# Optimization experiments

Measured on AMD Instinct MI355X. Metric: run time of the kernel, lower is better.

Reference implementation:

```python
import jax, jax.numpy as jnp
import numpy as np

N, E, IN, TD, H, C0, C1 = 50000, 800000, 128, 64, 4, 64, 16
SLOPE = 0.2


def setup_inputs() -> dict:
    key = jax.random.key(0)
    ks = jax.random.split(key, 20)
    def rn(k, shape, scale=1.0):
        return jax.random.normal(k, shape, dtype=jnp.float32) * scale
    return {
        "x": rn(ks[0], (N, IN)),
        "edge_index": jax.random.randint(ks[1], (2, E), 0, N),
        "timestamps": jax.random.uniform(ks[2], (E,), dtype=jnp.float32),
        # TimeEncoder: linear(1 -> TD) then cos, then abs
        "time_w": rn(ks[3], (TD,)),
        "time_b": rn(ks[4], (TD,)),
        # GATConv layer 0: in=IN, out-per-head=C0, heads=H
        "W0": rn(ks[5], (IN, H * C0), 0.1),
        "att_src0": rn(ks[6], (H, C0), 0.1),
        "att_dst0": rn(ks[7], (H, C0), 0.1),
        "lin_edge0": rn(ks[8], (TD, H * C0), 0.1),
        "att_edge0": rn(ks[9], (H, C0), 0.1),
        "bias0": rn(ks[10], (H * C0,), 0.1),
        # GATConv layer 1: in=H*C0, out-per-head=C1, heads=H
        "W1": rn(ks[11], (H * C0, H * C1), 0.1),
        "att_src1": rn(ks[12], (H, C1), 0.1),
        "att_dst1": rn(ks[13], (H, C1), 0.1),
        "lin_edge1": rn(ks[14], (TD, H * C1), 0.1),
        "att_edge1": rn(ks[15], (H, C1), 0.1),
        "bias1": rn(ks[16], (H * C1,), 0.1),
    }


def gat_layer(h_in, src, dst, edge_attr, W, a_src, a_dst, W_e, a_e, bias):
    """One PyG-style GATConv with edge-attr attention (concat heads, no dropout)."""
    heads = a_src.shape[0]
    HC = W.shape[1]
    C = HC // heads
    n_nodes = h_in.shape[0]
    h = (h_in @ W).reshape(n_nodes, heads, C)                 # [N, H, C]
    e = (edge_attr @ W_e).reshape(-1, heads, C)               # [Et, H, C]
    # attention logits per edge, per head
    alpha = ((h * a_src).sum(-1)[src]
             + (h * a_dst).sum(-1)[dst]
             + (e * a_e).sum(-1))                              # [Et, H]
    alpha = jnp.where(alpha >= 0, alpha, SLOPE * alpha)       # leaky relu
    # segment softmax over destination node
    m = jax.ops.segment_max(alpha, dst, num_segments=n_nodes)  # [N, H]
    ea = jnp.exp(alpha - m[dst])
    s = jax.ops.segment_sum(ea, dst, num_segments=n_nodes)
    a = ea / (s[dst] + 1e-16)                                 # [Et, H]
    # weighted scatter-add aggregation
    out = jax.ops.segment_sum(h[src] * a[..., None], dst, num_segments=n_nodes)
    return out.reshape(n_nodes, HC) + bias


def reference(x, edge_index, timestamps, time_w, time_b,
              W0, att_src0, att_dst0, lin_edge0, att_edge0, bias0,
              W1, att_src1, att_dst1, lin_edge1, att_edge1, bias1):
    # TimeEncoder -> abs, per-edge feature [E, TD]
    ef = jnp.abs(jnp.cos(timestamps[:, None] * time_w + time_b))
    # add self loops with edge_attr fill value 1.0
    loops = jnp.arange(N)
    src = jnp.concatenate([edge_index[0], loops])
    dst = jnp.concatenate([edge_index[1], loops])
    ef = jnp.concatenate([ef, jnp.ones((N, TD), ef.dtype)], axis=0)
    h = gat_layer(x, src, dst, ef, W0, att_src0, att_dst0, lin_edge0, att_edge0, bias0)
    h = gat_layer(h, src, dst, ef, W1, att_src1, att_dst1, lin_edge1, att_edge1, bias1)
    return h  # [N, H*C1] = [50000, 64]
```

## Files before the change

### kernel.cpp

```cpp
#include <hip/hip_runtime.h>
#include <math.h>

#define N_NODES 50000
#define N_EDGES 800000
#define ET (N_EDGES + N_NODES)
#define IN_F 128
#define TDIM 64
#define HEADS 4
#define C0 64
#define C1 16
#define HC0 256
#define HC1 64
#define KF 512
#define SLOPE 0.2f
#define TAB 4096
#define BSHIFT 7
#define NBUCKET 391
#define CHUNK 2048

using short8 = __attribute__((ext_vector_type(8))) short;
using f32x4 = __attribute__((ext_vector_type(4))) float;

__device__ __forceinline__ float bf2f(unsigned u16) { return __uint_as_float(u16 << 16); }
__device__ __forceinline__ unsigned short f2bf(float f) {
    unsigned u = __float_as_uint(f);
    return (unsigned short)((u + 0x7fffu + ((u >> 16) & 1u)) >> 16);
}
__device__ __forceinline__ unsigned pk2(float lo, float hi) {
    return (unsigned)f2bf(lo) | ((unsigned)f2bf(hi) << 16);
}
__device__ __forceinline__ float lrelu(float a) { return a >= 0.f ? a : SLOPE * a; }

__global__ __launch_bounds__(256) void k_param(
    const float* __restrict__ le0, const float* __restrict__ at0, const float* __restrict__ le1,
    const float* __restrict__ at1, const float* __restrict__ W0, const float* __restrict__ asr,
    const float* __restrict__ ads, const float* __restrict__ W1, const float* __restrict__ bias0,
    const float* __restrict__ asr1, const float* __restrict__ ads1,
    const float* __restrict__ tw, const float* __restrict__ tb, float* __restrict__ l0,
    float* __restrict__ l1, float* __restrict__ as0, float* __restrict__ ad0,
    unsigned short* __restrict__ W01t, float* __restrict__ b01, float* __restrict__ as1,
    float* __restrict__ ad1, float* __restrict__ bs1, float* __restrict__ bd1,
    float* __restrict__ tab0, float* __restrict__ tab1) {
    int b = blockIdx.x, tid = threadIdx.x;
    int h = tid >> 6, c = tid & 63;
    if (b == 0) {
        float s0 = 0.f;
        for (int td = 0; td < TDIM; ++td) s0 += le0[td * HC0 + h * C0 + c];
        s0 *= at0[h * C0 + c];
        for (int m = 1; m < 64; m <<= 1) s0 += __shfl_xor(s0, m);
        if (c == 0) l0[h] = s0;
        float s1 = 0.f;
        if (c < C1) {
            for (int td = 0; td < TDIM; ++td) s1 += le1[td * HC1 + h * C1 + c];
            s1 *= at1[h * C1 + c];
        }
        for (int m = 1; m < 16; m <<= 1) s1 += __shfl_xor(s1, m);
        if (c == 0) l1[h] = s1;
    } else if (b < 129) {
        int k = b - 1;
        float wv = W0[k * HC0 + h * C0 + c];
        float ps = wv * asr[h * C0 + c];
        float pd = wv * ads[h * C0 + c];
        for (int m = 1; m < 64; m <<= 1) {
            ps += __shfl_xor(ps, m);
            pd += __shfl_xor(pd, m);
        }
        if (c == 0) {
            as0[h * IN_F + k] = ps;
            ad0[h * IN_F + k] = pd;
        }
    } else if (b < 257) {
        int hk = (b - 129) * 4 + (tid >> 6);
        int c1 = tid & 63;
        int hh = hk >> 7, k = hk & 127;
        float acc = 0.f;
        for (int c0 = 0; c0 < C0; ++c0)
            acc += W0[k * HC0 + hh * C0 + c0] * W1[(size_t)(hh * C0 + c0) * HC1 + c1];
        W01t[(size_t)c1 * KF + hk] = f2bf(acc);
        float ps = acc * asr1[c1];
        float pd = acc * ads1[c1];
        for (int m = 1; m < 16; m <<= 1) {
            ps += __shfl_xor(ps, m);
            pd += __shfl_xor(pd, m);
        }
        if ((c1 & 15) == 0) {
            as1[(c1 >> 4) * KF + hk] = ps;
            ad1[(c1 >> 4) * KF + hk] = pd;
        }
    } else if (b == 257) {
        if (tid < 64) {
            float acc = 0.f;
            for (int k = 0; k < HC0; ++k) acc += bias0[k] * W1[(size_t)k * HC1 + tid];
            b01[tid] = acc;
            float ps = acc * asr1[tid];
            float pd = acc * ads1[tid];
            for (int m = 1; m < 16; m <<= 1) {
                ps += __shfl_xor(ps, m);
                pd += __shfl_xor(pd, m);
            }
            if ((tid & 15) == 0) {
                bs1[tid >> 4] = ps;
                bd1[tid >> 4] = pd;
            }
        }
    } else {
        __shared__ float sv0[TDIM * 4], sv1[TDIM * 4], sw[TDIM], sb[TDIM];
        int td = tid >> 2, hh = tid & 3;
        float v0l = 0.f;
        for (int c0 = 0; c0 < C0; ++c0) v0l += le0[td * HC0 + hh * C0 + c0] * at0[hh * C0 + c0];
        sv0[td * 4 + hh] = v0l;
        float v1l = 0.f;
        for (int c0 = 0; c0 < C1; ++c0) v1l += le1[td * HC1 + hh * C1 + c0] * at1[hh * C1 + c0];
        sv1[td * 4 + hh] = v1l;
        if (tid < TDIM) {
            sw[tid] = tw[tid];
            sb[tid] = tb[tid];
        }
        __syncthreads();
        int i = (b - 258) * 256 + tid;
        if (i > TAB) return;
        float time = (float)i / (float)TAB;
        float a00 = 0, a01 = 0, a02 = 0, a03 = 0, a10 = 0, a11 = 0, a12 = 0, a13 = 0;
#pragma unroll 8
        for (int d = 0; d < TDIM; ++d) {
            float f = fabsf(__cosf(time * sw[d] + sb[d]));
            a00 += f * sv0[d * 4 + 0];
            a01 += f * sv0[d * 4 + 1];
            a02 += f * sv0[d * 4 + 2];
            a03 += f * sv0[d * 4 + 3];
            a10 += f * sv1[d * 4 + 0];
            a11 += f * sv1[d * 4 + 1];
            a12 += f * sv1[d * 4 + 2];
            a13 += f * sv1[d * 4 + 3];
        }
        ((float4*)tab0)[i] = make_float4(a00, a01, a02, a03);
        ((float4*)tab1)[i] = make_float4(a10, a11, a12, a13);
    }
}

__global__ __launch_bounds__(256) void k_xbs(const float* __restrict__ x,
                                             const float* __restrict__ as0,
                                             const float* __restrict__ ad0,
                                             unsigned short* __restrict__ xb,
                                             float* __restrict__ ssrc, float* __restrict__ sdst,
                                             int* __restrict__ deg) {
    if (blockIdx.x < 196) {
        int i = blockIdx.x * 256 + threadIdx.x;
        if (i < N_NODES) deg[i] = 0;
    }
    int w = threadIdx.x >> 6, l = threadIdx.x & 63;
    int n = blockIdx.x * 4 + w;
    if (n >= N_NODES) return;
    float2 xv = *(const float2*)(x + (size_t)n * IN_F + l * 2);
    *(unsigned*)(xb + (size_t)n * IN_F + l * 2) = pk2(xv.x, xv.y);
    float ps[4], pd[4];
#pragma unroll
    for (int h = 0; h < 4; ++h) {
        float2 a = *(const float2*)(as0 + h * IN_F + l * 2);
        float2 d = *(const float2*)(ad0 + h * IN_F + l * 2);
        ps[h] = xv.x * a.x + xv.y * a.y;
        pd[h] = xv.x * d.x + xv.y * d.y;
    }
#pragma unroll
    for (int m = 1; m < 64; m <<= 1) {
#pragma unroll
        for (int h = 0; h < 4; ++h) {
            ps[h] += __shfl_xor(ps[h], m);
            pd[h] += __shfl_xor(pd[h], m);
        }
    }
    if (l == 0) {
#pragma unroll
        for (int h = 0; h < 4; ++h) {
            ssrc[n * 4 + h] = ps[h];
            sdst[n * 4 + h] = pd[h];
        }
    }
}

__global__ void k_count(const int* __restrict__ ei, int* __restrict__ deg) {
    int t = blockIdx.x * blockDim.x + threadIdx.x;
    if (t >= N_EDGES) return;
    atomicAdd(&deg[ei[N_EDGES + t]], 1);
}

__global__ void k_scan_block(const int* __restrict__ deg, int* __restrict__ rowptr,
                             int* __restrict__ blocksum, int n) {
    __shared__ int buf[256];
    int tid = threadIdx.x, i = blockIdx.x * 256 + tid;
    int v = (i < n) ? (deg[i] + 1) : 0;
    buf[tid] = v;
    __syncthreads();
    for (int off = 1; off < 256; off <<= 1) {
        int t = (tid >= off) ? buf[tid - off] : 0;
        __syncthreads();
        buf[tid] += t;
        __syncthreads();
    }
    if (i < n) rowptr[i + 1] = buf[tid];
    if (tid == 255) blocksum[blockIdx.x] = buf[255];
}

__global__ void k_scan_top(const int* __restrict__ blocksum, int* __restrict__ blockoff, int nb) {
    __shared__ int buf[256];
    int tid = threadIdx.x;
    int v = (tid < nb) ? blocksum[tid] : 0;
    buf[tid] = v;
    __syncthreads();
    for (int off = 1; off < 256; off <<= 1) {
        int t = (tid >= off) ? buf[tid - off] : 0;
        __syncthreads();
        buf[tid] += t;
        __syncthreads();
    }
    if (tid < nb) blockoff[tid] = buf[tid] - v;
}

__global__ void k_finalize(int* __restrict__ rowptr, const int* __restrict__ blockoff,
                           const int* __restrict__ deg, int* __restrict__ cursor,
                           int* __restrict__ edst, int* __restrict__ esrc,
                           float* __restrict__ tsp, int* __restrict__ bcur,
                           const float* __restrict__ ssrc0, const float* __restrict__ sdst0,
                           const float* __restrict__ l0, float* __restrict__ ew0p) {
    int i = blockIdx.x * 256 + threadIdx.x;
    if (i >= N_NODES) return;
    int v = rowptr[i + 1] + blockoff[blockIdx.x];
    rowptr[i + 1] = v;
    int start = v - deg[i] - 1;
    cursor[i] = start;
    if (i == 0) rowptr[0] = 0;
    if ((i & ((1 << BSHIFT) - 1)) == 0) bcur[i >> BSHIFT] = start;
    for (int p = start; p < v; ++p) edst[p] = i;
    esrc[v - 1] = i;
    tsp[v - 1] = -1.f;
    float4 lv = ((const float4*)l0)[0];
    float4 sv = ((const float4*)ssrc0)[i];
    float4 dv = ((const float4*)sdst0)[i];
    float4 w;
    w.x = __expf(lrelu(sv.x + dv.x + lv.x));
    w.y = __expf(lrelu(sv.y + dv.y + lv.y));
    w.z = __expf(lrelu(sv.z + dv.z + lv.z));
    w.w = __expf(lrelu(sv.w + dv.w + lv.w));
    ((float4*)ew0p)[v - 1] = w;
}

__global__ __launch_bounds__(256) void k_bucketA(const int* __restrict__ ei,
                                                 const float* __restrict__ ts,
                                                 int* __restrict__ bcur,
                                                 int4* __restrict__ staging) {
    __shared__ int cnt[NBUCKET], base[NBUCKET];
    int tid = threadIdx.x;
    int e0 = blockIdx.x * CHUNK;
    for (int i = tid; i < NBUCKET; i += 256) cnt[i] = 0;
    __syncthreads();
    int s[8], d[8], tv[8];
#pragma unroll
    for (int i = 0; i < 8; ++i) {
        int tt = e0 + i * 256 + tid;
        if (tt < N_EDGES) {
            s[i] = ei[tt];
            d[i] = ei[N_EDGES + tt];
            tv[i] = __float_as_int(ts[tt]);
            atomicAdd(&cnt[d[i] >> BSHIFT], 1);
        } else {
            d[i] = -1;
        }
    }
    __syncthreads();
    for (int i = tid; i < NBUCKET; i += 256) {
        int c = cnt[i];
        base[i] = c ? atomicAdd(&bcur[i], c) : 0;
        cnt[i] = 0;
    }
    __syncthreads();
#pragma unroll
    for (int i = 0; i < 8; ++i) {
        if (d[i] >= 0) {
            int b = d[i] >> BSHIFT;
            int off = atomicAdd(&cnt[b], 1);
            staging[base[b] + off] = make_int4(s[i], d[i], tv[i], 0);
        }
    }
}

__global__ __launch_bounds__(256) void k_bucketB(
    const int* __restrict__ rowptr, const int* __restrict__ bcur,
    const int4* __restrict__ staging, int* __restrict__ cursor, int* __restrict__ esrc,
    float* __restrict__ tsp, const float* __restrict__ ssrc0, const float* __restrict__ sdst0,
    const float* __restrict__ tab0, float* __restrict__ ew0p) {
    int b = blockIdx.x;
    int lo = rowptr[b << BSHIFT];
    int hi = bcur[b];
    for (int p = lo + threadIdx.x; p < hi; p += 256) {
        int4 sdt = staging[p];
        int q = atomicAdd(&cursor[sdt.y], 1);
        esrc[q] = sdt.x;
        float tv = __int_as_float(sdt.z);
        tsp[q] = tv;
        float f = tv * (float)TAB;
        int i = (int)f;
        i = i > TAB - 1 ? TAB - 1 : i;
        float fr = f - (float)i;
        float4 t0 = ((const float4*)tab0)[i];
        float4 t1 = ((const float4*)tab0)[i + 1];
        float4 sv = ((const float4*)ssrc0)[sdt.x];
        float4 dv = ((const float4*)sdst0)[sdt.y];
        float4 w;
        w.x = __expf(lrelu(sv.x + dv.x + t0.x + fr * (t1.x - t0.x)));
        w.y = __expf(lrelu(sv.y + dv.y + t0.y + fr * (t1.y - t0.y)));
        w.z = __expf(lrelu(sv.z + dv.z + t0.z + fr * (t1.z - t0.z)));
        w.w = __expf(lrelu(sv.w + dv.w + t0.w + fr * (t1.w - t0.w)));
        ((float4*)ew0p)[q] = w;
    }
}

__global__ void k_ew1(const int* __restrict__ esrc, const int* __restrict__ edst,
                      const float* __restrict__ tsp, const float* __restrict__ tab1,
                      const float* __restrict__ l1, const float* __restrict__ ssrc,
                      const float* __restrict__ sdst, float* __restrict__ ew1p) {
    int p = blockIdx.x * blockDim.x + threadIdx.x;
    if (p >= ET) return;
    float tv = tsp[p];
    float4 av;
    if (tv < 0.f) {
        av = ((const float4*)l1)[0];
    } else {
        float f = tv * (float)TAB;
        int i = (int)f;
        i = i > TAB - 1 ? TAB - 1 : i;
        float fr = f - (float)i;
        float4 t0 = ((const float4*)tab1)[i];
        float4 t1 = ((const float4*)tab1)[i + 1];
        av.x = t0.x + fr * (t1.x - t0.x);
        av.y = t0.y + fr * (t1.y - t0.y);
        av.z = t0.z + fr * (t1.z - t0.z);
        av.w = t0.w + fr * (t1.w - t0.w);
    }
    int s = esrc[p], d = edst[p];
    float4 sv = ((const float4*)ssrc)[s];
    float4 dv = ((const float4*)sdst)[d];
    float4 w;
    w.x = __expf(lrelu(sv.x + dv.x + av.x));
    w.y = __expf(lrelu(sv.y + dv.y + av.y));
    w.z = __expf(lrelu(sv.z + dv.z + av.z));
    w.w = __expf(lrelu(sv.w + dv.w + av.w));
    ((float4*)ew1p)[p] = w;
}

__global__ __launch_bounds__(256) void k_aggx(
    const unsigned short* __restrict__ xb, const int* __restrict__ esrc,
    const float* __restrict__ ew0p, const int* __restrict__ rowptr,
    const float* __restrict__ as1, const float* __restrict__ ad1,
    const float* __restrict__ bs1, const float* __restrict__ bd1,
    unsigned short* __restrict__ aggx, float* __restrict__ ssrc1, float* __restrict__ sdst1) {
    int grp = threadIdx.x >> 4, lo = threadIdx.x & 15;
    int n = blockIdx.x * 16 + grp;
    if (n >= N_NODES) return;
    int p0 = rowptr[n], p1 = rowptr[n + 1];
    float acc[4][8];
#pragma unroll
    for (int h = 0; h < 4; ++h)
#pragma unroll
        for (int j = 0; j < 8; ++j) acc[h][j] = 0.f;
    float ss0 = 0, ss1 = 0, ss2 = 0, ss3 = 0;
    float4 e_cur = ((const float4*)ew0p)[p0];
    uint4 x_cur = *(const uint4*)(xb + (size_t)esrc[p0] * IN_F + lo * 8);
    int s_nxt = (p0 + 1 < p1) ? esrc[p0 + 1] : 0;
    for (int p = p0; p < p1; ++p) {
        float4 e = e_cur;
        uint4 xv = x_cur;
        if (p + 1 < p1) {
            e_cur = ((const float4*)ew0p)[p + 1];
            x_cur = *(const uint4*)(xb + (size_t)s_nxt * IN_F + lo * 8);
            if (p + 2 < p1) s_nxt = esrc[p + 2];
        }
        float f[8];
        f[0] = bf2f(xv.x & 0xffff);
        f[1] = bf2f(xv.x >> 16);
        f[2] = bf2f(xv.y & 0xffff);
        f[3] = bf2f(xv.y >> 16);
        f[4] = bf2f(xv.z & 0xffff);
        f[5] = bf2f(xv.z >> 16);
        f[6] = bf2f(xv.w & 0xffff);
        f[7] = bf2f(xv.w >> 16);
#pragma unroll
        for (int j = 0; j < 8; ++j) {
            acc[0][j] += e.x * f[j];
            acc[1][j] += e.y * f[j];
            acc[2][j] += e.z * f[j];
            acc[3][j] += e.w * f[j];
        }
        ss0 += e.x;
        ss1 += e.y;
        ss2 += e.z;
        ss3 += e.w;
    }
    float inv[4] = {1.f / (ss0 + 1e-16f), 1.f / (ss1 + 1e-16f), 1.f / (ss2 + 1e-16f),
                    1.f / (ss3 + 1e-16f)};
    size_t base = (size_t)n * KF + lo * 8;
    float ps[4] = {0, 0, 0, 0}, pd[4] = {0, 0, 0, 0};
#pragma unroll
    for (int h = 0; h < 4; ++h) {
        float av[8];
#pragma unroll
        for (int j = 0; j < 8; ++j) av[j] = acc[h][j] * inv[h];
        uint4 r;
        r.x = pk2(av[0], av[1]);
        r.y = pk2(av[2], av[3]);
        r.z = pk2(av[4], av[5]);
        r.w = pk2(av[6], av[7]);
        *(uint4*)(aggx + base + h * IN_F) = r;
        int hkb = h * IN_F + lo * 8;
#pragma unroll
        for (int hs = 0; hs < 4; ++hs) {
            float4 a0 = *(const float4*)(as1 + hs * KF + hkb);
            float4 a1 = *(const float4*)(as1 + hs * KF + hkb + 4);
            float4 d0 = *(const float4*)(ad1 + hs * KF + hkb);
            float4 d1 = *(const float4*)(ad1 + hs * KF + hkb + 4);
            ps[hs] += av[0] * a0.x + av[1] * a0.y + av[2] * a0.z + av[3] * a0.w + av[4] * a1.x +
                      av[5] * a1.y + av[6] * a1.z + av[7] * a1.w;
            pd[hs] += av[0] * d0.x + av[1] * d0.y + av[2] * d0.z + av[3] * d0.w + av[4] * d1.x +
                      av[5] * d1.y + av[6] * d1.z + av[7] * d1.w;
        }
    }
#pragma unroll
    for (int m = 1; m < 16; m <<= 1) {
#pragma unroll
        for (int hs = 0; hs < 4; ++hs) {
            ps[hs] += __shfl_xor(ps[hs], m);
            pd[hs] += __shfl_xor(pd[hs], m);
        }
    }
    if (lo == 0) {
#pragma unroll
        for (int hs = 0; hs < 4; ++hs) {
            ssrc1[n * 4 + hs] = ps[hs] + bs1[hs];
            sdst1[n * 4 + hs] = pd[hs] + bd1[hs];
        }
    }
}

__global__ __launch_bounds__(256) void k_gemm1(const unsigned short* __restrict__ A,
                                               const unsigned short* __restrict__ Bt,
                                               const float* __restrict__ b01,
                                               unsigned short* __restrict__ h1b) {
    __shared__ unsigned short As[128 * 40];
    __shared__ unsigned short Bs[64 * 40];
    int tid = threadIdx.x, w = tid >> 6, l = tid & 63, lo = l & 15, hi = l >> 4;
    int m0 = blockIdx.x * 128;
    f32x4 acc[2][4];
#pragma unroll
    for (int i = 0; i < 2; ++i)
#pragma unroll
        for (int j = 0; j < 4; ++j) acc[i][j] = (f32x4){0.f, 0.f, 0.f, 0.f};
    int arow4 = tid >> 2, aseg = tid & 3;
    for (int k0 = 0; k0 < KF; k0 += 32) {
#pragma unroll
        for (int hf = 0; hf < 2; ++hf) {
            int arow = hf * 64 + arow4;
            uint4 va = {0, 0, 0, 0};
            if (m0 + arow < N_NODES)
                va = *(const uint4*)(A + (size_t)(m0 + arow) * KF + k0 + aseg * 8);
            *(uint4*)&As[arow * 40 + aseg * 8] = va;
        }
        uint4 vb = *(const uint4*)(Bt + (size_t)arow4 * KF + k0 + aseg * 8);
        *(uint4*)&Bs[arow4 * 40 + aseg * 8] = vb;
        __syncthreads();
        short8 af[2], bf[4];
#pragma unroll
        for (int fa = 0; fa < 2; ++fa)
            af[fa] = *(const short8*)&As[(w * 32 + fa * 16 + lo) * 40 + hi * 8];
#pragma unroll
        for (int nf = 0; nf < 4; ++nf) bf[nf] = *(const short8*)&Bs[(nf * 16 + lo) * 40 + hi * 8];
#pragma unroll
        for (int fa = 0; fa < 2; ++fa)
#pragma unroll
            for (int nf = 0; nf < 4; ++nf)
                acc[fa][nf] =
                    __builtin_amdgcn_mfma_f32_16x16x32_bf16(af[fa], bf[nf], acc[fa][nf], 0, 0, 0);
        __syncthreads();
    }
#pragma unroll
    for (int fa = 0; fa < 2; ++fa)
#pragma unroll
        for (int nf = 0; nf < 4; ++nf) {
            int col = nf * 16 + lo;
            float bv = b01[col];
#pragma unroll
            for (int r = 0; r < 4; ++r) {
                int row = m0 + w * 32 + fa * 16 + hi * 4 + r;
                if (row < N_NODES) h1b[(size_t)row * HC1 + col] = f2bf(acc[fa][nf][r] + bv);
            }
        }
}

__global__ __launch_bounds__(256) void k_agg1(
    const unsigned short* __restrict__ h1b, const int* __restrict__ esrc,
    const float* __restrict__ ew1p, const int* __restrict__ rowptr,
    const float* __restrict__ bias, float* __restrict__ out) {
    int grp = threadIdx.x >> 4, lo = threadIdx.x & 15;
    int n = blockIdx.x * 16 + grp;
    if (n >= N_NODES) return;
    int head = lo >> 2;
    int p0 = rowptr[n], p1 = rowptr[n + 1];
    float a0 = 0, a1 = 0, a2 = 0, a3 = 0, ss = 0;
    float e_cur = ew1p[p0 * 4 + head];
    uint2 h_cur = *(const uint2*)(h1b + (size_t)esrc[p0] * HC1 + lo * 4);
    for (int p = p0; p < p1; ++p) {
        float e = e_cur;
        uint2 hv = h_cur;
        if (p + 1 < p1) {
            e_cur = ew1p[(p + 1) * 4 + head];
            h_cur = *(const uint2*)(h1b + (size_t)esrc[p + 1] * HC1 + lo * 4);
        }
        a0 += e * bf2f(hv.x & 0xffff);
        a1 += e * bf2f(hv.x >> 16);
        a2 += e * bf2f(hv.y & 0xffff);
        a3 += e * bf2f(hv.y >> 16);
        ss += e;
    }
    float inv = 1.f / (ss + 1e-16f);
    float4 b4 = *(const float4*)(bias + lo * 4);
    float4 r = make_float4(a0 * inv + b4.x, a1 * inv + b4.y, a2 * inv + b4.z, a3 * inv + b4.w);
    *(float4*)(out + (size_t)n * HC1 + lo * 4) = r;
}

extern "C" void kernel_launch(void* const* d_in, const int* in_sizes, int n_in, void* d_out,
                              int out_size, void* d_ws, size_t ws_size, hipStream_t stream) {
    const float* x = (const float*)d_in[0];
    const int* ei = (const int*)d_in[1];
    const float* ts = (const float*)d_in[2];
    const float* time_w = (const float*)d_in[3];
    const float* time_b = (const float*)d_in[4];
    const float* W0 = (const float*)d_in[5];
    const float* att_src0 = (const float*)d_in[6];
    const float* att_dst0 = (const float*)d_in[7];
    const float* lin_edge0 = (const float*)d_in[8];
    const float* att_edge0 = (const float*)d_in[9];
    const float* bias0 = (const float*)d_in[10];
    const float* W1 = (const float*)d_in[11];
    const float* att_src1 = (const float*)d_in[12];
    const float* att_dst1 = (const float*)d_in[13];
    const float* lin_edge1 = (const float*)d_in[14];
    const float* att_edge1 = (const float*)d_in[15];
    const float* bias1 = (const float*)d_in[16];
    float* out = (float*)d_out;

    char* ws = (char*)d_ws;
    size_t off = 0;
    auto alloc = [&](size_t bytes) -> void* {
        void* p = ws + off;
        off = (off + bytes + 255) & ~(size_t)255;
        return p;
    };
    unsigned short* xb = (unsigned short*)alloc((size_t)N_NODES * IN_F * 2);
    unsigned short* aggx = (unsigned short*)alloc((size_t)N_NODES * KF * 2);
    unsigned short* h1b = (unsigned short*)alloc((size_t)N_NODES * HC1 * 2);
    unsigned short* W01t = (unsigned short*)alloc((size_t)HC1 * KF * 2);
    float* b01 = (float*)alloc(HC1 * 4);
    float* as0 = (float*)alloc(4 * IN_F * 4);
    float* ad0 = (float*)alloc(4 * IN_F * 4);
    float* as1 = (float*)alloc(4 * KF * 4);
    float* ad1 = (float*)alloc(4 * KF * 4);
    float* bs1 = (float*)alloc(16);
    float* bd1 = (float*)alloc(16);
    float* tab0 = (float*)alloc((size_t)(TAB + 1) * 4 * 4);
    float* tab1 = (float*)alloc((size_t)(TAB + 1) * 4 * 4);
    float* ew0p = (float*)alloc((size_t)ET * 4 * 4);
    float* ew1p = (float*)alloc((size_t)ET * 4 * 4);
    float* ssrc0 = (float*)alloc((size_t)N_NODES * 4 * 4);
    float* sdst0 = (float*)alloc((size_t)N_NODES * 4 * 4);
    float* ssrc1 = (float*)alloc((size_t)N_NODES * 4 * 4);
    float* sdst1 = (float*)alloc((size_t)N_NODES * 4 * 4);
    float* l0 = (float*)alloc(16);
    float* l1 = (float*)alloc(16);
    float* tsp = (float*)alloc((size_t)ET * 4);
    int* deg = (int*)alloc((size_t)N_NODES * 4);
    int* rowptr = (int*)alloc((size_t)(N_NODES + 1) * 4);
    int* cursor = (int*)alloc((size_t)(N_NODES + 1) * 4);
    int* blocksum = (int*)alloc(256 * 4);
    int* blockoff = (int*)alloc(256 * 4);
    int* bcur = (int*)alloc(NBUCKET * 4);
    int4* staging = (int4*)alloc((size_t)ET * 16);
    int* esrc = (int*)alloc((size_t)ET * 4);
    int* edst = (int*)alloc((size_t)ET * 4);
    (void)ws_size;
    (void)in_sizes;
    (void)n_in;
    (void)out_size;

    int nb = (N_NODES + 255) / 256;
    int ebks = (ET + 255) / 256;
    int rbks = (N_EDGES + 255) / 256;
    int cbks = (N_EDGES + CHUNK - 1) / CHUNK;
    int gx = (N_NODES + 127) / 128;
    int nblk16 = (N_NODES + 15) / 16;
    int nblk4 = (N_NODES + 3) / 4;

    k_param<<<275, 256, 0, stream>>>(lin_edge0, att_edge0, lin_edge1, att_edge1, W0, att_src0,
                                     att_dst0, W1, bias0, att_src1, att_dst1, time_w, time_b, l0,
                                     l1, as0, ad0, W01t, b01, as1, ad1, bs1, bd1, tab0, tab1);

    k_xbs<<<nblk4, 256, 0, stream>>>(x, as0, ad0, xb, ssrc0, sdst0, deg);

    k_count<<<rbks, 256, 0, stream>>>(ei, deg);
    k_scan_block<<<nb, 256, 0, stream>>>(deg, rowptr, blocksum, N_NODES);
    k_scan_top<<<1, 256, 0, stream>>>(blocksum, blockoff, nb);
    k_finalize<<<nb, 256, 0, stream>>>(rowptr, blockoff, deg, cursor, edst, esrc, tsp, bcur,
                                       ssrc0, sdst0, l0, ew0p);
    k_bucketA<<<cbks, 256, 0, stream>>>(ei, ts, bcur, staging);
    k_bucketB<<<NBUCKET, 256, 0, stream>>>(rowptr, bcur, staging, cursor, esrc, tsp, ssrc0, sdst0,
                                           tab0, ew0p);

    k_aggx<<<nblk16, 256, 0, stream>>>(xb, esrc, ew0p, rowptr, as1, ad1, bs1, bd1, aggx, ssrc1,
                                       sdst1);

    k_ew1<<<ebks, 256, 0, stream>>>(esrc, edst, tsp, tab1, l1, ssrc1, sdst1, ew1p);
    k_gemm1<<<gx, 256, 0, stream>>>(aggx, W01t, b01, h1b);
    k_agg1<<<nblk16, 256, 0, stream>>>(h1b, esrc, ew1p, rowptr, bias1, out);
}
```

Measured before the change: 262.7 us.

## Compute layer-1 attention scores in GEMM epilogue instead of aggregation kernel

Layer-1 source/destination attention scores were previously computed in the aggregation kernel from the bf16-rounded aggregated features against precomputed projected attention vectors. They are now computed in the epilogue of the layer-1 GEMM as dot products of the output features with att_src1/att_dst1, using 16-lane shuffle reductions. The GEMM is moved ahead of the edge-weight kernel because of the new dependency. This removes per-node extra loads and FMAs from the aggregation kernel and drops the precomputed vectors from the parameter kernel. In exchange the GEMM epilogue gains many shuffle reductions, and the scores now come from GEMM outputs that use bf16-rounded inputs.

```diff
diff --git a/kernel.cpp b/kernel.cpp
--- a/kernel.cpp
+++ b/kernel.cpp
@@ -35,12 +35,10 @@
     const float* __restrict__ le0, const float* __restrict__ at0, const float* __restrict__ le1,
     const float* __restrict__ at1, const float* __restrict__ W0, const float* __restrict__ asr,
     const float* __restrict__ ads, const float* __restrict__ W1, const float* __restrict__ bias0,
-    const float* __restrict__ asr1, const float* __restrict__ ads1,
     const float* __restrict__ tw, const float* __restrict__ tb, float* __restrict__ l0,
     float* __restrict__ l1, float* __restrict__ as0, float* __restrict__ ad0,
-    unsigned short* __restrict__ W01t, float* __restrict__ b01, float* __restrict__ as1,
-    float* __restrict__ ad1, float* __restrict__ bs1, float* __restrict__ bd1,
-    float* __restrict__ tab0, float* __restrict__ tab1) {
+    unsigned short* __restrict__ W01t, float* __restrict__ b01, float* __restrict__ tab0,
+    float* __restrict__ tab1) {
     int b = blockIdx.x, tid = threadIdx.x;
     int h = tid >> 6, c = tid & 63;
     if (b == 0) {
@@ -77,31 +75,11 @@
         for (int c0 = 0; c0 < C0; ++c0)
             acc += W0[k * HC0 + hh * C0 + c0] * W1[(size_t)(hh * C0 + c0) * HC1 + c1];
         W01t[(size_t)c1 * KF + hk] = f2bf(acc);
-        float ps = acc * asr1[c1];
-        float pd = acc * ads1[c1];
-        for (int m = 1; m < 16; m <<= 1) {
-            ps += __shfl_xor(ps, m);
-            pd += __shfl_xor(pd, m);
-        }
-        if ((c1 & 15) == 0) {
-            as1[(c1 >> 4) * KF + hk] = ps;
-            ad1[(c1 >> 4) * KF + hk] = pd;
-        }
     } else if (b == 257) {
         if (tid < 64) {
             float acc = 0.f;
             for (int k = 0; k < HC0; ++k) acc += bias0[k] * W1[(size_t)k * HC1 + tid];
             b01[tid] = acc;
-            float ps = acc * asr1[tid];
-            float pd = acc * ads1[tid];
-            for (int m = 1; m < 16; m <<= 1) {
-                ps += __shfl_xor(ps, m);
-                pd += __shfl_xor(pd, m);
-            }
-            if ((tid & 15) == 0) {
-                bs1[tid >> 4] = ps;
-                bd1[tid >> 4] = pd;
-            }
         }
     } else {
         __shared__ float sv0[TDIM * 4], sv1[TDIM * 4], sw[TDIM], sb[TDIM];
@@ -347,12 +325,11 @@
     ((float4*)ew1p)[p] = w;
 }
 
-__global__ __launch_bounds__(256) void k_aggx(
-    const unsigned short* __restrict__ xb, const int* __restrict__ esrc,
-    const float* __restrict__ ew0p, const int* __restrict__ rowptr,
-    const float* __restrict__ as1, const float* __restrict__ ad1,
-    const float* __restrict__ bs1, const float* __restrict__ bd1,
-    unsigned short* __restrict__ aggx, float* __restrict__ ssrc1, float* __restrict__ sdst1) {
+__global__ __launch_bounds__(256) void k_aggx(const unsigned short* __restrict__ xb,
+                                              const int* __restrict__ esrc,
+                                              const float* __restrict__ ew0p,
+                                              const int* __restrict__ rowptr,
+                                              unsigned short* __restrict__ aggx) {
     int grp = threadIdx.x >> 4, lo = threadIdx.x & 15;
     int n = blockIdx.x * 16 + grp;
     if (n >= N_NODES) return;
@@ -398,52 +375,22 @@
     float inv[4] = {1.f / (ss0 + 1e-16f), 1.f / (ss1 + 1e-16f), 1.f / (ss2 + 1e-16f),
                     1.f / (ss3 + 1e-16f)};
     size_t base = (size_t)n * KF + lo * 8;
-    float ps[4] = {0, 0, 0, 0}, pd[4] = {0, 0, 0, 0};
 #pragma unroll
     for (int h = 0; h < 4; ++h) {
-        float av[8];
-#pragma unroll
-        for (int j = 0; j < 8; ++j) av[j] = acc[h][j] * inv[h];
         uint4 r;
-        r.x = pk2(av[0], av[1]);
-        r.y = pk2(av[2], av[3]);
-        r.z = pk2(av[4], av[5]);
-        r.w = pk2(av[6], av[7]);
+        r.x = pk2(acc[h][0] * inv[h], acc[h][1] * inv[h]);
+        r.y = pk2(acc[h][2] * inv[h], acc[h][3] * inv[h]);
+        r.z = pk2(acc[h][4] * inv[h], acc[h][5] * inv[h]);
+        r.w = pk2(acc[h][6] * inv[h], acc[h][7] * inv[h]);
         *(uint4*)(aggx + base + h * IN_F) = r;
-        int hkb = h * IN_F + lo * 8;
-#pragma unroll
-        for (int hs = 0; hs < 4; ++hs) {
-            float4 a0 = *(const float4*)(as1 + hs * KF + hkb);
-            float4 a1 = *(const float4*)(as1 + hs * KF + hkb + 4);
-            float4 d0 = *(const float4*)(ad1 + hs * KF + hkb);
-            float4 d1 = *(const float4*)(ad1 + hs * KF + hkb + 4);
-            ps[hs] += av[0] * a0.x + av[1] * a0.y + av[2] * a0.z + av[3] * a0.w + av[4] * a1.x +
-                      av[5] * a1.y + av[6] * a1.z + av[7] * a1.w;
-            pd[hs] += av[0] * d0.x + av[1] * d0.y + av[2] * d0.z + av[3] * d0.w + av[4] * d1.x +
-                      av[5] * d1.y + av[6] * d1.z + av[7] * d1.w;
-        }
-    }
-#pragma unroll
-    for (int m = 1; m < 16; m <<= 1) {
-#pragma unroll
-        for (int hs = 0; hs < 4; ++hs) {
-            ps[hs] += __shfl_xor(ps[hs], m);
-            pd[hs] += __shfl_xor(pd[hs], m);
-        }
-    }
-    if (lo == 0) {
-#pragma unroll
-        for (int hs = 0; hs < 4; ++hs) {
-            ssrc1[n * 4 + hs] = ps[hs] + bs1[hs];
-            sdst1[n * 4 + hs] = pd[hs] + bd1[hs];
-        }
-    }
-}
-
-__global__ __launch_bounds__(256) void k_gemm1(const unsigned short* __restrict__ A,
-                                               const unsigned short* __restrict__ Bt,
-                                               const float* __restrict__ b01,
-                                               unsigned short* __restrict__ h1b) {
+    }
+}
+
+__global__ __launch_bounds__(256) void k_gemm1s(
+    const unsigned short* __restrict__ A, const unsigned short* __restrict__ Bt,
+    const float* __restrict__ b01, const float* __restrict__ a_src,
+    const float* __restrict__ a_dst, unsigned short* __restrict__ h1b, float* __restrict__ ssrc,
+    float* __restrict__ sdst) {
     __shared__ unsigned short As[128 * 40];
     __shared__ unsigned short Bs[64 * 40];
     int tid = threadIdx.x, w = tid >> 6, l = tid & 63, lo = l & 15, hi = l >> 4;
@@ -480,16 +427,31 @@
                     __builtin_amdgcn_mfma_f32_16x16x32_bf16(af[fa], bf[nf], acc[fa][nf], 0, 0, 0);
         __syncthreads();
     }
+    float asv[4], adv[4], bv[4];
+#pragma unroll
+    for (int nf = 0; nf < 4; ++nf) {
+        asv[nf] = a_src[nf * 16 + lo];
+        adv[nf] = a_dst[nf * 16 + lo];
+        bv[nf] = b01[nf * 16 + lo];
+    }
 #pragma unroll
     for (int fa = 0; fa < 2; ++fa)
 #pragma unroll
-        for (int nf = 0; nf < 4; ++nf) {
-            int col = nf * 16 + lo;
-            float bv = b01[col];
-#pragma unroll
-            for (int r = 0; r < 4; ++r) {
-                int row = m0 + w * 32 + fa * 16 + hi * 4 + r;
-                if (row < N_NODES) h1b[(size_t)row * HC1 + col] = f2bf(acc[fa][nf][r] + bv);
+        for (int r = 0; r < 4; ++r) {
+            int row = m0 + w * 32 + fa * 16 + hi * 4 + r;
+#pragma unroll
+            for (int nf = 0; nf < 4; ++nf) {
+                float v = acc[fa][nf][r] + bv[nf];
+                if (row < N_NODES) h1b[(size_t)row * HC1 + nf * 16 + lo] = f2bf(v);
+                float ps = v * asv[nf], pd = v * adv[nf];
+                for (int m = 1; m < 16; m <<= 1) {
+                    ps += __shfl_xor(ps, m);
+                    pd += __shfl_xor(pd, m);
+                }
+                if (lo == 0 && row < N_NODES) {
+                    ssrc[row * 4 + nf] = ps;
+                    sdst[row * 4 + nf] = pd;
+                }
             }
         }
 }
@@ -560,10 +522,6 @@
     float* b01 = (float*)alloc(HC1 * 4);
     float* as0 = (float*)alloc(4 * IN_F * 4);
     float* ad0 = (float*)alloc(4 * IN_F * 4);
-    float* as1 = (float*)alloc(4 * KF * 4);
-    float* ad1 = (float*)alloc(4 * KF * 4);
-    float* bs1 = (float*)alloc(16);
-    float* bd1 = (float*)alloc(16);
     float* tab0 = (float*)alloc((size_t)(TAB + 1) * 4 * 4);
     float* tab1 = (float*)alloc((size_t)(TAB + 1) * 4 * 4);
     float* ew0p = (float*)alloc((size_t)ET * 4 * 4);
@@ -598,8 +556,8 @@
     int nblk4 = (N_NODES + 3) / 4;
 
     k_param<<<275, 256, 0, stream>>>(lin_edge0, att_edge0, lin_edge1, att_edge1, W0, att_src0,
-                                     att_dst0, W1, bias0, att_src1, att_dst1, time_w, time_b, l0,
-                                     l1, as0, ad0, W01t, b01, as1, ad1, bs1, bd1, tab0, tab1);
+                                     att_dst0, W1, bias0, time_w, time_b, l0, l1, as0, ad0, W01t,
+                                     b01, tab0, tab1);
 
     k_xbs<<<nblk4, 256, 0, stream>>>(x, as0, ad0, xb, ssrc0, sdst0, deg);
 
@@ -612,10 +570,9 @@
     k_bucketB<<<NBUCKET, 256, 0, stream>>>(rowptr, bcur, staging, cursor, esrc, tsp, ssrc0, sdst0,
                                            tab0, ew0p);
 
-    k_aggx<<<nblk16, 256, 0, stream>>>(xb, esrc, ew0p, rowptr, as1, ad1, bs1, bd1, aggx, ssrc1,
-                                       sdst1);
-
+    k_aggx<<<nblk16, 256, 0, stream>>>(xb, esrc, ew0p, rowptr, aggx);
+
+    k_gemm1s<<<gx, 256, 0, stream>>>(aggx, W01t, b01, att_src1, att_dst1, h1b, ssrc1, sdst1);
     k_ew1<<<ebks, 256, 0, stream>>>(esrc, edst, tsp, tab1, l1, ssrc1, sdst1, ew1p);
-    k_gemm1<<<gx, 256, 0, stream>>>(aggx, W01t, b01, h1b);
     k_agg1<<<nblk16, 256, 0, stream>>>(h1b, esrc, ew1p, rowptr, bias1, out);
 }
```

Result: faster. 246.7 us (-6.1%).
